# Performance work log

Measured on AMD Instinct MI355X. Metric: run time of the kernel, lower is better.

The kernel has to match this reference:

```python
import jax, jax.numpy as jnp
import numpy as np

KERNEL_SIZE = 3
ITERATIONS = 4


def _box_conv(x, kernel):
    # x: [B,1,H,W], kernel: [1,1,k,k]; SAME padding via pad=(k-1)//2
    p = (KERNEL_SIZE - 1) // 2
    return jax.lax.conv_general_dilated(
        x, kernel,
        window_strides=(1, 1),
        padding=((p, p), (p, p)),
        dimension_numbers=("NCHW", "OIHW", "NCHW"),
    )


def setup_inputs() -> dict:
    key = jax.random.key(0)
    inputs = jax.random.uniform(key, (32, 1, 512, 512), dtype=jnp.float32)
    return {"inputs": inputs}


def reference(inputs) -> jnp.ndarray:
    # fixed box-filter kernel: every tap = 1/k^2, bias = 0 (frozen in torch module)
    kernel = jnp.full((1, 1, KERNEL_SIZE, KERNEL_SIZE), 1.0 / KERNEL_SIZE**2, dtype=inputs.dtype)
    blob = inputs
    for _ in range(ITERATIONS):
        # NOTE: original module convolves `inputs` (not previous blob) each iteration
        blob = _box_conv(inputs, kernel)
        blob = jax.nn.sigmoid((blob - 0.01) * 1000.0)
        blob = _box_conv(blob, kernel)
        blob = jax.nn.sigmoid((blob - 0.9) * 1000.0)
    return blob
```

## Files before the change

kernel.cpp:

```cpp
#include <hip/hip_runtime.h>


#define IMG 512
#define BH  8
#define NROWS (BH + 4)
#define NIT   (BH + 2)

__device__ __forceinline__ float steep_sig(float sum9, float bias) {
    float x = fmaf(sum9, 1000.0f / 9.0f, bias);
    return __builtin_amdgcn_rcpf(1.0f + __expf(-x));
}

__device__ __forceinline__ float4 f4add3(float4 a, float4 b, float4 c) {
    return make_float4(a.x + b.x + c.x, a.y + b.y + c.y,
                       a.z + b.z + c.z, a.w + b.w + c.w);
}

__global__ __launch_bounds__(256) void blobber_fused(const float* __restrict__ in,
                                                     float* __restrict__ out) {
    const int tid  = threadIdx.x;
    const int lane = tid & 63;
    const int gw   = blockIdx.x * 4 + (tid >> 6);
    const int band = gw & 63;
    const int img  = gw >> 6;
    const int y0   = band * BH;

    const int colL = 4 * lane;
    const int colR = 256 + 4 * lane;

    const float* ip = in  + (size_t)img * (IMG * IMG);
    float*       op = out + (size_t)img * (IMG * IMG);

    float4 inL[NROWS], inR[NROWS];
    #pragma unroll
    for (int k = 0; k < NROWS; ++k) {
        const int r = y0 - 2 + k;
        inL[k] = make_float4(0.f, 0.f, 0.f, 0.f);
        inR[k] = make_float4(0.f, 0.f, 0.f, 0.f);
        if ((unsigned)r < IMG) {
            inL[k] = *(const float4*)(ip + r * IMG + colL);
            inR[k] = *(const float4*)(ip + r * IMG + colR);
        }
    }

    const float4 z4 = make_float4(0.f, 0.f, 0.f, 0.f);
    float4 h2mL = z4, h2cL = z4, h2mR = z4, h2cR = z4;

    #pragma unroll
    for (int s = 0; s < NIT; ++s) {
        const int r = y0 - 1 + s;

        float4 vL = f4add3(inL[s], inL[s + 1], inL[s + 2]);
        float4 vR = f4add3(inR[s], inR[s + 1], inR[s + 2]);

        float Llft = __shfl_up(vL.w, 1);
        float Lrgt = __shfl_down(vL.x, 1);
        float Rlft = __shfl_up(vR.w, 1);
        float Rrgt = __shfl_down(vR.x, 1);
        float c256 = __shfl(vR.x, 0);
        float c255 = __shfl(vL.w, 63);
        if (lane == 0)  { Llft = 0.0f;  Rlft = c255; }
        if (lane == 63) { Lrgt = c256;  Rrgt = 0.0f; }

        float4 s1L, s1R;
        if ((unsigned)r < IMG) {
            s1L.x = steep_sig(Llft + vL.x + vL.y, -10.0f);
            s1L.y = steep_sig(vL.x + vL.y + vL.z, -10.0f);
            s1L.z = steep_sig(vL.y + vL.z + vL.w, -10.0f);
            s1L.w = steep_sig(vL.z + vL.w + Lrgt, -10.0f);
            s1R.x = steep_sig(Rlft + vR.x + vR.y, -10.0f);
            s1R.y = steep_sig(vR.x + vR.y + vR.z, -10.0f);
            s1R.z = steep_sig(vR.y + vR.z + vR.w, -10.0f);
            s1R.w = steep_sig(vR.z + vR.w + Rrgt, -10.0f);
        } else {
            s1L = z4; s1R = z4;
        }

        float sLl = __shfl_up(s1L.w, 1);
        float sLr = __shfl_down(s1L.x, 1);
        float sRl = __shfl_up(s1R.w, 1);
        float sRr = __shfl_down(s1R.x, 1);
        float s256 = __shfl(s1R.x, 0);
        float s255 = __shfl(s1L.w, 63);
        if (lane == 0)  { sLl = 0.0f;  sRl = s255; }
        if (lane == 63) { sLr = s256;  sRr = 0.0f; }

        float4 h2pL, h2pR;
        h2pL.x = sLl   + s1L.x + s1L.y;
        h2pL.y = s1L.x + s1L.y + s1L.z;
        h2pL.z = s1L.y + s1L.z + s1L.w;
        h2pL.w = s1L.z + s1L.w + sLr;
        h2pR.x = sRl   + s1R.x + s1R.y;
        h2pR.y = s1R.x + s1R.y + s1R.z;
        h2pR.z = s1R.y + s1R.z + s1R.w;
        h2pR.w = s1R.z + s1R.w + sRr;

        if (s >= 2) {
            const int oy = r - 1;
            float4 oL, oR;
            oL.x = steep_sig(h2mL.x + h2cL.x + h2pL.x, -900.0f);
            oL.y = steep_sig(h2mL.y + h2cL.y + h2pL.y, -900.0f);
            oL.z = steep_sig(h2mL.z + h2cL.z + h2pL.z, -900.0f);
            oL.w = steep_sig(h2mL.w + h2cL.w + h2pL.w, -900.0f);
            oR.x = steep_sig(h2mR.x + h2cR.x + h2pR.x, -900.0f);
            oR.y = steep_sig(h2mR.y + h2cR.y + h2pR.y, -900.0f);
            oR.z = steep_sig(h2mR.z + h2cR.z + h2pR.z, -900.0f);
            oR.w = steep_sig(h2mR.w + h2cR.w + h2pR.w, -900.0f);
            *(float4*)(op + oy * IMG + colL) = oL;
            *(float4*)(op + oy * IMG + colR) = oR;
        }

        h2mL = h2cL; h2cL = h2pL;
        h2mR = h2cR; h2cR = h2pR;
    }
}

extern "C" void kernel_launch(void* const* d_in, const int* in_sizes, int n_in,
                              void* d_out, int out_size, void* d_ws, size_t ws_size,
                              hipStream_t stream) {
    const float* in  = (const float*)d_in[0];
    float*       out = (float*)d_out;
    blobber_fused<<<dim3(512), dim3(256), 0, stream>>>(in, out);
}
```

Before: 83.91 us.

## Halve row band height, double waves, use contiguous 8-column lane layout

Each wavefront now computes a 4-row band instead of an 8-row band, so twice as many blocks launch (1024). Each lane now owns 8 contiguous columns instead of two separate groups of 4, which cuts the shuffles per stage from six to two. A launch-bounds occupancy hint is also added. The goal is to raise the number of waves per CU to hide latency in this latency-bound fused kernel. The cost is more redundant halo row loads and recomputed first-stage rows per output row, and less regular coalescing per load instruction.

```diff
diff --git a/kernel.cpp b/kernel.cpp
--- a/kernel.cpp
+++ b/kernel.cpp
@@ -2,9 +2,9 @@
 
 
 #define IMG 512
-#define BH  8
-#define NROWS (BH + 4)
-#define NIT   (BH + 2)
+#define BH  4
+#define NR  (BH + 4)
+#define NIT (BH + 2)
 
 __device__ __forceinline__ float steep_sig(float sum9, float bias) {
     float x = fmaf(sum9, 1000.0f / 9.0f, bias);
@@ -16,102 +16,94 @@
                        a.z + b.z + c.z, a.w + b.w + c.w);
 }
 
-__global__ __launch_bounds__(256) void blobber_fused(const float* __restrict__ in,
-                                                     float* __restrict__ out) {
+__global__ __launch_bounds__(256, 4) void blobber_fused(const float* __restrict__ in,
+                                                        float* __restrict__ out) {
     const int tid  = threadIdx.x;
     const int lane = tid & 63;
     const int gw   = blockIdx.x * 4 + (tid >> 6);
-    const int band = gw & 63;
-    const int img  = gw >> 6;
+    const int band = gw & 127;
+    const int img  = gw >> 7;
     const int y0   = band * BH;
-
-    const int colL = 4 * lane;
-    const int colR = 256 + 4 * lane;
+    const int xA   = 8 * lane;
 
     const float* ip = in  + (size_t)img * (IMG * IMG);
     float*       op = out + (size_t)img * (IMG * IMG);
 
-    float4 inL[NROWS], inR[NROWS];
+    float4 A[NR], B[NR];
     #pragma unroll
-    for (int k = 0; k < NROWS; ++k) {
+    for (int k = 0; k < NR; ++k) {
         const int r = y0 - 2 + k;
-        inL[k] = make_float4(0.f, 0.f, 0.f, 0.f);
-        inR[k] = make_float4(0.f, 0.f, 0.f, 0.f);
+        A[k] = make_float4(0.f, 0.f, 0.f, 0.f);
+        B[k] = make_float4(0.f, 0.f, 0.f, 0.f);
         if ((unsigned)r < IMG) {
-            inL[k] = *(const float4*)(ip + r * IMG + colL);
-            inR[k] = *(const float4*)(ip + r * IMG + colR);
+            const float* row = ip + r * IMG + xA;
+            A[k] = *(const float4*)(row);
+            B[k] = *(const float4*)(row + 4);
         }
     }
 
     const float4 z4 = make_float4(0.f, 0.f, 0.f, 0.f);
-    float4 h2mL = z4, h2cL = z4, h2mR = z4, h2cR = z4;
+    float4 h2mA = z4, h2mB = z4, h2cA = z4, h2cB = z4;
 
     #pragma unroll
     for (int s = 0; s < NIT; ++s) {
         const int r = y0 - 1 + s;
 
-        float4 vL = f4add3(inL[s], inL[s + 1], inL[s + 2]);
-        float4 vR = f4add3(inR[s], inR[s + 1], inR[s + 2]);
+        float4 vA = f4add3(A[s], A[s + 1], A[s + 2]);
+        float4 vB = f4add3(B[s], B[s + 1], B[s + 2]);
 
-        float Llft = __shfl_up(vL.w, 1);
-        float Lrgt = __shfl_down(vL.x, 1);
-        float Rlft = __shfl_up(vR.w, 1);
-        float Rrgt = __shfl_down(vR.x, 1);
-        float c256 = __shfl(vR.x, 0);
-        float c255 = __shfl(vL.w, 63);
-        if (lane == 0)  { Llft = 0.0f;  Rlft = c255; }
-        if (lane == 63) { Lrgt = c256;  Rrgt = 0.0f; }
+        float lft = __shfl_up(vB.w, 1);
+        float rgt = __shfl_down(vA.x, 1);
+        if (lane == 0)  lft = 0.0f;
+        if (lane == 63) rgt = 0.0f;
 
-        float4 s1L, s1R;
+        float4 s1A, s1B;
         if ((unsigned)r < IMG) {
-            s1L.x = steep_sig(Llft + vL.x + vL.y, -10.0f);
-            s1L.y = steep_sig(vL.x + vL.y + vL.z, -10.0f);
-            s1L.z = steep_sig(vL.y + vL.z + vL.w, -10.0f);
-            s1L.w = steep_sig(vL.z + vL.w + Lrgt, -10.0f);
-            s1R.x = steep_sig(Rlft + vR.x + vR.y, -10.0f);
-            s1R.y = steep_sig(vR.x + vR.y + vR.z, -10.0f);
-            s1R.z = steep_sig(vR.y + vR.z + vR.w, -10.0f);
-            s1R.w = steep_sig(vR.z + vR.w + Rrgt, -10.0f);
+            s1A.x = steep_sig(lft  + vA.x + vA.y, -10.0f);
+            s1A.y = steep_sig(vA.x + vA.y + vA.z, -10.0f);
+            s1A.z = steep_sig(vA.y + vA.z + vA.w, -10.0f);
+            s1A.w = steep_sig(vA.z + vA.w + vB.x, -10.0f);
+            s1B.x = steep_sig(vA.w + vB.x + vB.y, -10.0f);
+            s1B.y = steep_sig(vB.x + vB.y + vB.z, -10.0f);
+            s1B.z = steep_sig(vB.y + vB.z + vB.w, -10.0f);
+            s1B.w = steep_sig(vB.z + vB.w + rgt,  -10.0f);
         } else {
-            s1L = z4; s1R = z4;
+            s1A = z4; s1B = z4;
         }
 
-        float sLl = __shfl_up(s1L.w, 1);
-        float sLr = __shfl_down(s1L.x, 1);
-        float sRl = __shfl_up(s1R.w, 1);
-        float sRr = __shfl_down(s1R.x, 1);
-        float s256 = __shfl(s1R.x, 0);
-        float s255 = __shfl(s1L.w, 63);
-        if (lane == 0)  { sLl = 0.0f;  sRl = s255; }
-        if (lane == 63) { sLr = s256;  sRr = 0.0f; }
+        float slft = __shfl_up(s1B.w, 1);
+        float srgt = __shfl_down(s1A.x, 1);
+        if (lane == 0)  slft = 0.0f;
+        if (lane == 63) srgt = 0.0f;
 
-        float4 h2pL, h2pR;
-        h2pL.x = sLl   + s1L.x + s1L.y;
-        h2pL.y = s1L.x + s1L.y + s1L.z;
-        h2pL.z = s1L.y + s1L.z + s1L.w;
-        h2pL.w = s1L.z + s1L.w + sLr;
-        h2pR.x = sRl   + s1R.x + s1R.y;
-        h2pR.y = s1R.x + s1R.y + s1R.z;
-        h2pR.z = s1R.y + s1R.z + s1R.w;
-        h2pR.w = s1R.z + s1R.w + sRr;
+        float4 h2pA, h2pB;
+        h2pA.x = slft  + s1A.x + s1A.y;
+        h2pA.y = s1A.x + s1A.y + s1A.z;
+        h2pA.z = s1A.y + s1A.z + s1A.w;
+        h2pA.w = s1A.z + s1A.w + s1B.x;
+        h2pB.x = s1A.w + s1B.x + s1B.y;
+        h2pB.y = s1B.x + s1B.y + s1B.z;
+        h2pB.z = s1B.y + s1B.z + s1B.w;
+        h2pB.w = s1B.z + s1B.w + srgt;
 
         if (s >= 2) {
             const int oy = r - 1;
-            float4 oL, oR;
-            oL.x = steep_sig(h2mL.x + h2cL.x + h2pL.x, -900.0f);
-            oL.y = steep_sig(h2mL.y + h2cL.y + h2pL.y, -900.0f);
-            oL.z = steep_sig(h2mL.z + h2cL.z + h2pL.z, -900.0f);
-            oL.w = steep_sig(h2mL.w + h2cL.w + h2pL.w, -900.0f);
-            oR.x = steep_sig(h2mR.x + h2cR.x + h2pR.x, -900.0f);
-            oR.y = steep_sig(h2mR.y + h2cR.y + h2pR.y, -900.0f);
-            oR.z = steep_sig(h2mR.z + h2cR.z + h2pR.z, -900.0f);
-            oR.w = steep_sig(h2mR.w + h2cR.w + h2pR.w, -900.0f);
-            *(float4*)(op + oy * IMG + colL) = oL;
-            *(float4*)(op + oy * IMG + colR) = oR;
+            float4 oA, oB;
+            oA.x = steep_sig(h2mA.x + h2cA.x + h2pA.x, -900.0f);
+            oA.y = steep_sig(h2mA.y + h2cA.y + h2pA.y, -900.0f);
+            oA.z = steep_sig(h2mA.z + h2cA.z + h2pA.z, -900.0f);
+            oA.w = steep_sig(h2mA.w + h2cA.w + h2pA.w, -900.0f);
+            oB.x = steep_sig(h2mB.x + h2cB.x + h2pB.x, -900.0f);
+            oB.y = steep_sig(h2mB.y + h2cB.y + h2pB.y, -900.0f);
+            oB.z = steep_sig(h2mB.z + h2cB.z + h2pB.z, -900.0f);
+            oB.w = steep_sig(h2mB.w + h2cB.w + h2pB.w, -900.0f);
+            float* orow = op + oy * IMG + xA;
+            *(float4*)(orow)     = oA;
+            *(float4*)(orow + 4) = oB;
         }
 
-        h2mL = h2cL; h2cL = h2pL;
-        h2mR = h2cR; h2cR = h2pR;
+        h2mA = h2cA; h2mB = h2cB;
+        h2cA = h2pA; h2cB = h2pB;
     }
 }
 
@@ -120,5 +112,5 @@
                               hipStream_t stream) {
     const float* in  = (const float*)d_in[0];
     float*       out = (float*)d_out;
-    blobber_fused<<<dim3(512), dim3(256), 0, stream>>>(in, out);
+    blobber_fused<<<dim3(1024), dim3(256), 0, stream>>>(in, out);
 }
```

Result: no change. 84.11 us (+0.2%).
